# Optimization experiments

Measured on AMD Instinct MI355X. Metric: run time of the kernel, lower is better.

## Reference

```python
import jax, jax.numpy as jnp
import numpy as np

N, D, H = 16384, 128, 512
C = 1.0          # curvature c_in
EPS_GIN = 0.0    # GIN epsilon
MIN_NORM = 1e-7


def _arcosh(z):
    z = jnp.clip(z, 1.0 + MIN_NORM, None)
    return jnp.log(z + jnp.sqrt(z * z - 1.0))


def exp_map_zero(u, c):
    # hyperboloid exp at origin; tangent 'time' coord u[...,0] is ignored
    sqrtK = 1.0 / jnp.sqrt(c)
    x = u[..., 1:]
    n = jnp.clip(jnp.linalg.norm(x, axis=-1, keepdims=True), MIN_NORM, None)
    theta = n / sqrtK
    return jnp.concatenate(
        [sqrtK * jnp.cosh(theta), sqrtK * jnp.sinh(theta) * x / n], axis=-1)


def log_map_zero(p, c):
    # hyperboloid log at origin; result has zero 'time' coord
    sqrtK = 1.0 / jnp.sqrt(c)
    y = p[..., 1:]
    n = jnp.clip(jnp.linalg.norm(y, axis=-1, keepdims=True), MIN_NORM, None)
    theta = _arcosh(p[..., :1] / sqrtK)
    return jnp.concatenate(
        [jnp.zeros_like(theta), sqrtK * theta * y / n], axis=-1)


def setup_inputs() -> dict:
    key = jax.random.key(0)
    k1, k2, k3, k4 = jax.random.split(key, 4)
    x = jax.random.normal(k1, (N, D), dtype=jnp.float32)
    adj = jax.random.uniform(k2, (N, N), dtype=jnp.float32) / N  # row-normalized-ish
    W1 = jax.random.normal(k3, (D, H), dtype=jnp.float32) * (1.0 / np.sqrt(D))
    b1 = jnp.zeros((H,), dtype=jnp.float32)
    W2 = jax.random.normal(k4, (H, D), dtype=jnp.float32) * (1.0 / np.sqrt(H))
    b2 = jnp.zeros((D,), dtype=jnp.float32)
    return {"x": x, "adj": adj, "W1": W1, "b1": b1, "W2": W2, "b2": b2}


def reference(x, adj, W1, b1, W2, b2):
    # 1) lift features onto hyperboloid
    h = exp_map_zero(x, C)                       # [N, D]
    # 2) LorentzAgg (no attention): aggregate in tangent space at origin
    agg = exp_map_zero(adj @ log_map_zero(h, C), C)   # [N, D]
    # 3) GIN combine in tangent space: log(out) + (1+eps)*log(x_r), then exp
    out = exp_map_zero(log_map_zero(agg, C) + (1.0 + EPS_GIN) * log_map_zero(h, C), C)
    # 4) GIN MLP
    t = jax.nn.relu(out @ W1 + b1) @ W2 + b2     # [N, D]
    return t
```

## Files before the change

### kernel.cpp

```cpp
#include <hip/hip_runtime.h>

#define GN 16384
#define GD 128
#define GH 512
#define GK 16384

#define SPLITS 4
#define SKK (GK / SPLITS)
#define BM 128
#define BK 64

typedef __attribute__((ext_vector_type(8))) short s8v;
typedef __attribute__((ext_vector_type(4))) float f4v;
typedef __attribute__((ext_vector_type(4))) int   i4v;

#define AS1 __attribute__((address_space(1)))
#define AS3 __attribute__((address_space(3)))

static __device__ inline unsigned short f2bf(float f) {
  union { float f; unsigned u; } a; a.f = f;
  unsigned r = a.u + 0x7fffu + ((a.u >> 16) & 1u);
  return (unsigned short)(r >> 16);
}

static __device__ inline unsigned cvtpk(float lo, float hi) {
  unsigned r;
  asm("v_cvt_pk_bf16_f32 %0, %1, %2" : "=v"(r) : "v"(lo), "v"(hi));
  return r;
}

static __device__ inline float waveAllSum(float v) {
  #pragma unroll
  for (int off = 32; off; off >>= 1) v += __shfl_xor(v, off);
  return v;
}

__global__ void k_logmap(const float* __restrict__ x, float* __restrict__ Lf) {
  int row  = (blockIdx.x << 2) + (threadIdx.x >> 6);
  int lane = threadIdx.x & 63;
  size_t base = ((size_t)row << 7) + (lane << 1);
  float2 v = *(const float2*)(x + base);
  float a0 = (lane == 0) ? 0.f : v.x;
  float a1 = v.y;
  float n = fmaxf(sqrtf(waveAllSum(a0*a0 + a1*a1)), 1e-7f);
  float sh = sinhf(n), ch = coshf(n);
  float y0 = sh * a0 / n, y1 = sh * a1 / n;
  float ny = fmaxf(sqrtf(waveAllSum(y0*y0 + y1*y1)), 1e-7f);
  float z  = fmaxf(ch, 1.f + 1e-7f);
  float th = logf(z + sqrtf(z*z - 1.f));
  float l0 = th * y0 / ny;
  float l1 = th * y1 / ny;
  if (lane == 0) l0 = 0.f;
  *(float2*)(Lf + base) = make_float2(l0, l1);
}

__global__ void k_tconv(const float* __restrict__ src, unsigned short* __restrict__ dst,
                        int NR, int NC) {
  __shared__ float tile[64][65];
  const int r0 = blockIdx.x << 6;
  const int c0 = blockIdx.y << 6;
  const int t  = threadIdx.x;
  const int r  = t >> 2;
  const int cg = (t & 3) << 4;
  const float* s = src + (size_t)(r0 + r) * NC + c0 + cg;
  #pragma unroll
  for (int j = 0; j < 4; ++j) {
    float4 f = ((const float4*)s)[j];
    tile[r][cg + 4*j + 0] = f.x;
    tile[r][cg + 4*j + 1] = f.y;
    tile[r][cg + 4*j + 2] = f.z;
    tile[r][cg + 4*j + 3] = f.w;
  }
  __syncthreads();
  s8v o0, o1;
  #pragma unroll
  for (int j = 0; j < 8; ++j) o0[j] = (short)f2bf(tile[cg + j][r]);
  #pragma unroll
  for (int j = 0; j < 8; ++j) o1[j] = (short)f2bf(tile[cg + 8 + j][r]);
  unsigned short* d = dst + (size_t)(c0 + r) * NR + r0 + cg;
  *(s8v*)d = o0;
  *((s8v*)d + 1) = o1;
}

__global__ __launch_bounds__(512) void k_gemm(const float* __restrict__ adj,
    const unsigned short* __restrict__ Lt, float* __restrict__ Mpart) {
  __shared__ __align__(16) float          As[BM * BK];
  __shared__ __align__(16) unsigned short Bs[128 * BK];
  const int tid  = threadIdx.x;
  const int lane = tid & 63, wid = tid >> 6;
  const int wr = wid >> 2, wn = wid & 3;
  const int l15 = lane & 15, lhi = (lane >> 4) << 3;
  const int bid = blockIdx.x;
  const int split = bid & 3, rowblk = bid >> 2;
  const size_t blockRow = (size_t)rowblk * BM;
  const size_t k0 = (size_t)split * SKK;

  f4v acc[4][2];
  #pragma unroll
  for (int m = 0; m < 4; ++m)
    #pragma unroll
    for (int n = 0; n < 2; ++n) acc[m][n] = (f4v){0.f, 0.f, 0.f, 0.f};

  const int rA = tid >> 4, gA = tid & 15;
  const float* aSrc = adj + (blockRow + rA) * (size_t)GK + k0
                      + (size_t)((gA ^ (rA & 7)) << 2);
  const int rB = tid >> 3, gB = tid & 7;
  const unsigned short* bSrc = Lt + (size_t)rB * GK + k0
                               + (size_t)((gB ^ (rB & 7)) << 3);

  char* AsB = (char*)As;
  char* BsB = (char*)Bs;

  const int NIT = SKK / BK;
  for (int it = 0; it < NIT; ++it) {
    const float*          ap = aSrc + (size_t)it * BK;
    const unsigned short* bp = bSrc + (size_t)it * BK;
    #pragma unroll
    for (int j = 0; j < 4; ++j)
      __builtin_amdgcn_global_load_lds(
        (const AS1 void*)(ap + (size_t)j * 32 * GK),
        (AS3 void*)(AsB + ((tid + j * 512) << 4)), 16, 0, 0);
    #pragma unroll
    for (int j = 0; j < 2; ++j)
      __builtin_amdgcn_global_load_lds(
        (const AS1 void*)(bp + (size_t)j * 64 * GK),
        (AS3 void*)(BsB + ((tid + j * 512) << 4)), 16, 0, 0);
    __syncthreads();

    #pragma unroll
    for (int ks = 0; ks < 2; ++ks) {
      s8v bfr[2];
      #pragma unroll
      for (int n = 0; n < 2; ++n) {
        int rowb = 32*wn + 16*n + l15;
        int gb   = (4*ks + (lhi >> 3)) ^ (rowb & 7);
        bfr[n] = *(const s8v*)(BsB + rowb * 128 + (gb << 4));
      }
      #pragma unroll
      for (int m = 0; m < 4; ++m) {
        int rowa = 64*wr + 16*m + l15;
        int ga0  = 8*ks + (lhi >> 2);
        int sw   = rowa & 7;
        f4v x0 = *(const f4v*)(AsB + rowa * 256 + ((ga0       ^ sw) << 4));
        f4v x1 = *(const f4v*)(AsB + rowa * 256 + (((ga0 + 1) ^ sw) << 4));
        union { unsigned u[4]; s8v v; } ua;
        ua.u[0] = cvtpk(x0[0], x0[1]);
        ua.u[1] = cvtpk(x0[2], x0[3]);
        ua.u[2] = cvtpk(x1[0], x1[1]);
        ua.u[3] = cvtpk(x1[2], x1[3]);
        acc[m][0] = __builtin_amdgcn_mfma_f32_16x16x32_bf16(ua.v, bfr[0], acc[m][0], 0, 0, 0);
        acc[m][1] = __builtin_amdgcn_mfma_f32_16x16x32_bf16(ua.v, bfr[1], acc[m][1], 0, 0, 0);
      }
    }
    __syncthreads();
  }

  float* mp = Mpart + (size_t)split * GN * GD;
  #pragma unroll
  for (int m = 0; m < 4; ++m)
    #pragma unroll
    for (int n = 0; n < 2; ++n) {
      size_t r0 = blockRow + 64*wr + 16*m + ((lane >> 4) << 2);
      int    c0 = 32*wn + 16*n + l15;
      #pragma unroll
      for (int j = 0; j < 4; ++j)
        mp[(r0 + j) * GD + c0] = acc[m][n][j];
    }
}

__global__ void k_maps(const float* __restrict__ Mp, const float* __restrict__ Lf,
                       unsigned short* __restrict__ outB) {
  int row  = (blockIdx.x << 2) + (threadIdx.x >> 6);
  int lane = threadIdx.x & 63;
  size_t base = ((size_t)row << 7) + (lane << 1);
  const size_t PS = (size_t)GN * GD;
  float2 m0 = *(const float2*)(Mp + base);
  float2 m1 = *(const float2*)(Mp + PS + base);
  float2 m2 = *(const float2*)(Mp + 2*PS + base);
  float2 m3 = *(const float2*)(Mp + 3*PS + base);
  float mvx = (m0.x + m1.x) + (m2.x + m3.x);
  float mvy = (m0.y + m1.y) + (m2.y + m3.y);
  float2 lv = *(const float2*)(Lf + base);
  float v0 = (lane == 0) ? 0.f : mvx;
  float v1 = mvy;
  float nv = fmaxf(sqrtf(waveAllSum(v0*v0 + v1*v1)), 1e-7f);
  float ch = coshf(nv), sh = sinhf(nv);
  float g0 = sh * v0 / nv, g1 = sh * v1 / nv;
  float ny = fmaxf(sqrtf(waveAllSum(g0*g0 + g1*g1)), 1e-7f);
  float z  = fmaxf(ch, 1.f + 1e-7f);
  float th = logf(z + sqrtf(z*z - 1.f));
  float la0 = th * g0 / ny, la1 = th * g1 / ny;
  float s0 = la0 + lv.x, s1 = la1 + lv.y;
  if (lane == 0) s0 = 0.f;
  float ns  = fmaxf(sqrtf(waveAllSum(s0*s0 + s1*s1)), 1e-7f);
  float ch2 = coshf(ns), sh2 = sinhf(ns);
  float o0 = sh2 * s0 / ns, o1 = sh2 * s1 / ns;
  if (lane == 0) o0 = ch2;
  unsigned pack = (unsigned)f2bf(o0) | ((unsigned)f2bf(o1) << 16);
  *(unsigned*)(outB + base) = pack;
}

#define PAD1 136
#define PADH 520
__global__ __launch_bounds__(256, 2) void k_mlp(const unsigned short* __restrict__ outB,
    const unsigned short* __restrict__ W1t, const float* __restrict__ b1,
    const unsigned short* __restrict__ W2t, const float* __restrict__ b2,
    float* __restrict__ Tout) {
  __shared__ __align__(16) short sA[32 * PAD1];
  __shared__ __align__(16) short sH[32 * PADH];
  const int tid  = threadIdx.x;
  const int lane = tid & 63, wc = tid >> 6;
  const int row0 = blockIdx.x << 5;

  {
    const int r = tid >> 3, cg = (tid & 7) << 4;
    const unsigned short* src = outB + (size_t)(row0 + r) * GD + cg;
    i4v v0 = ((const i4v*)src)[0];
    i4v v1 = ((const i4v*)src)[1];
    *(i4v*)&sA[r * PAD1 + cg]     = v0;
    *(i4v*)&sA[r * PAD1 + cg + 8] = v1;
  }
  __syncthreads();

  f4v acc1[2][8];
  #pragma unroll
  for (int mi = 0; mi < 2; ++mi)
    #pragma unroll
    for (int ni = 0; ni < 8; ++ni) acc1[mi][ni] = (f4v){0.f,0.f,0.f,0.f};

  const int afr = (lane & 15) * PAD1 + ((lane >> 4) << 3);
  #pragma unroll
  for (int kk = 0; kk < 4; ++kk) {
    s8v a0 = *(const s8v*)&sA[afr + kk*32];
    s8v a1 = *(const s8v*)&sA[afr + 16*PAD1 + kk*32];
    #pragma unroll
    for (int ni = 0; ni < 8; ++ni) {
      const unsigned short* bp = W1t + (size_t)(128*wc + 16*ni + (lane & 15)) * GD
                                 + ((lane >> 4) << 3) + kk*32;
      s8v b = *(const s8v*)bp;
      acc1[0][ni] = __builtin_amdgcn_mfma_f32_16x16x32_bf16(a0, b, acc1[0][ni], 0, 0, 0);
      acc1[1][ni] = __builtin_amdgcn_mfma_f32_16x16x32_bf16(a1, b, acc1[1][ni], 0, 0, 0);
    }
  }
  #pragma unroll
  for (int ni = 0; ni < 8; ++ni) {
    int col = 128*wc + 16*ni + (lane & 15);
    float bb = b1[col];
    #pragma unroll
    for (int mi = 0; mi < 2; ++mi) {
      #pragma unroll
      for (int j = 0; j < 4; ++j) {
        int row = 16*mi + ((lane >> 4) << 2) + j;
        float v = fmaxf(acc1[mi][ni][j] + bb, 0.f);
        sH[row * PADH + col] = (short)f2bf(v);
      }
    }
  }
  __syncthreads();

  f4v acc2[2][2];
  #pragma unroll
  for (int mi = 0; mi < 2; ++mi)
    #pragma unroll
    for (int ni = 0; ni < 2; ++ni) acc2[mi][ni] = (f4v){0.f,0.f,0.f,0.f};

  const int hfr = (lane & 15) * PADH + ((lane >> 4) << 3);
  #pragma unroll
  for (int kk = 0; kk < 16; ++kk) {
    s8v a0 = *(const s8v*)&sH[hfr + kk*32];
    s8v a1 = *(const s8v*)&sH[hfr + 16*PADH + kk*32];
    #pragma unroll
    for (int ni = 0; ni < 2; ++ni) {
      const unsigned short* bp = W2t + (size_t)(32*wc + 16*ni + (lane & 15)) * GH
                                 + ((lane >> 4) << 3) + kk*32;
      s8v b = *(const s8v*)bp;
      acc2[0][ni] = __builtin_amdgcn_mfma_f32_16x16x32_bf16(a0, b, acc2[0][ni], 0, 0, 0);
      acc2[1][ni] = __builtin_amdgcn_mfma_f32_16x16x32_bf16(a1, b, acc2[1][ni], 0, 0, 0);
    }
  }
  #pragma unroll
  for (int mi = 0; mi < 2; ++mi)
    #pragma unroll
    for (int ni = 0; ni < 2; ++ni) {
      int c0 = 32*wc + 16*ni + (lane & 15);
      float bb = b2[c0];
      size_t r0 = row0 + 16*mi + ((lane >> 4) << 2);
      #pragma unroll
      for (int j = 0; j < 4; ++j)
        Tout[(r0 + j) * GD + c0] = acc2[mi][ni][j] + bb;
    }
}

extern "C" void kernel_launch(void* const* d_in, const int* in_sizes, int n_in,
                              void* d_out, int out_size, void* d_ws, size_t ws_size,
                              hipStream_t stream) {
  const float* x   = (const float*)d_in[0];
  const float* adj = (const float*)d_in[1];
  const float* W1  = (const float*)d_in[2];
  const float* b1  = (const float*)d_in[3];
  const float* W2  = (const float*)d_in[4];
  const float* b2  = (const float*)d_in[5];
  float* Tout = (float*)d_out;

  char* ws = (char*)d_ws;
  float*          Lf    = (float*)ws;
  unsigned short* Lt    = (unsigned short*)(ws + (8u  << 20));
  float*          Mpart = (float*)(ws + (12u << 20));
  unsigned short* outB  = (unsigned short*)(ws + (44u << 20));
  unsigned short* W1t   = (unsigned short*)(ws + (48u << 20));
  unsigned short* W2t   = (unsigned short*)(ws + (48u << 20) + (128u << 10));

  k_logmap <<<GN / 4, 256, 0, stream>>>(x, Lf);
  k_tconv  <<<dim3(GK / 64, GD / 64), 256, 0, stream>>>(Lf, Lt, GN, GD);
  k_tconv  <<<dim3(GD / 64, GH / 64), 256, 0, stream>>>(W1, W1t, GD, GH);
  k_tconv  <<<dim3(GH / 64, GD / 64), 256, 0, stream>>>(W2, W2t, GH, GD);
  k_gemm   <<<(GN / BM) * SPLITS, 512, 0, stream>>>(adj, Lt, Mpart);
  k_maps   <<<GN / 4, 256, 0, stream>>>(Mpart, Lf, outB);
  k_mlp    <<<GN / 32, 256, 0, stream>>>(outB, W1t, b1, W2t, b2, Tout);
}
```

Before: 274.7 us.

## Double-buffer adjacency GEMM LDS stages with smaller row tiles and fewer K splits

The adj@L GEMM now uses two LDS buffers so global-to-LDS loads for the next K step are issued before computing the current one. Row tiles shrink from 128 to 64 and K splits drop from 4 to 2, keeping the block count while halving the partial-sum buffers written and reduced in the maps kernel. The trade-off is twice the reads of the transposed L matrix and higher LDS use per block, which may limit occupancy.

```diff
diff --git a/kernel.cpp b/kernel.cpp
--- a/kernel.cpp
+++ b/kernel.cpp
@@ -5,9 +5,9 @@
 #define GH 512
 #define GK 16384
 
-#define SPLITS 4
+#define SPLITS 2
 #define SKK (GK / SPLITS)
-#define BM 128
+#define BM 64
 #define BK 64
 
 typedef __attribute__((ext_vector_type(8))) short s8v;
@@ -82,22 +82,24 @@
   *((s8v*)d + 1) = o1;
 }
 
+#define ASZ (BM * BK * 4)
+#define BSZ (128 * BK * 2)
+#define BUFSZ (ASZ + BSZ)
 __global__ __launch_bounds__(512) void k_gemm(const float* __restrict__ adj,
     const unsigned short* __restrict__ Lt, float* __restrict__ Mpart) {
-  __shared__ __align__(16) float          As[BM * BK];
-  __shared__ __align__(16) unsigned short Bs[128 * BK];
+  __shared__ __align__(16) char lds[2 * BUFSZ];
   const int tid  = threadIdx.x;
   const int lane = tid & 63, wid = tid >> 6;
   const int wr = wid >> 2, wn = wid & 3;
   const int l15 = lane & 15, lhi = (lane >> 4) << 3;
   const int bid = blockIdx.x;
-  const int split = bid & 3, rowblk = bid >> 2;
+  const int split = bid & 1, rowblk = bid >> 1;
   const size_t blockRow = (size_t)rowblk * BM;
   const size_t k0 = (size_t)split * SKK;
 
-  f4v acc[4][2];
-  #pragma unroll
-  for (int m = 0; m < 4; ++m)
+  f4v acc[2][2];
+  #pragma unroll
+  for (int m = 0; m < 2; ++m)
     #pragma unroll
     for (int n = 0; n < 2; ++n) acc[m][n] = (f4v){0.f, 0.f, 0.f, 0.f};
 
@@ -108,25 +110,35 @@
   const unsigned short* bSrc = Lt + (size_t)rB * GK + k0
                                + (size_t)((gB ^ (rB & 7)) << 3);
 
-  char* AsB = (char*)As;
-  char* BsB = (char*)Bs;
-
   const int NIT = SKK / BK;
+
+#define STAGE(c, itv)                                                          \
+  {                                                                            \
+    const float*          ap = aSrc + (size_t)(itv) * BK;                      \
+    const unsigned short* bp = bSrc + (size_t)(itv) * BK;                      \
+    char* ab = lds + (c) * BUFSZ;                                              \
+    char* bb = lds + (c) * BUFSZ + ASZ;                                        \
+    _Pragma("unroll")                                                          \
+    for (int j = 0; j < 2; ++j)                                                \
+      __builtin_amdgcn_global_load_lds(                                        \
+        (const AS1 void*)(ap + (size_t)j * 32 * GK),                           \
+        (AS3 void*)(ab + ((tid + j * 512) << 4)), 16, 0, 0);                   \
+    _Pragma("unroll")                                                          \
+    for (int j = 0; j < 2; ++j)                                                \
+      __builtin_amdgcn_global_load_lds(                                        \
+        (const AS1 void*)(bp + (size_t)j * 64 * GK),                           \
+        (AS3 void*)(bb + ((tid + j * 512) << 4)), 16, 0, 0);                   \
+  }
+
+  int cur = 0;
+  STAGE(0, 0);
+  __syncthreads();
+
   for (int it = 0; it < NIT; ++it) {
-    const float*          ap = aSrc + (size_t)it * BK;
-    const unsigned short* bp = bSrc + (size_t)it * BK;
-    #pragma unroll
-    for (int j = 0; j < 4; ++j)
-      __builtin_amdgcn_global_load_lds(
-        (const AS1 void*)(ap + (size_t)j * 32 * GK),
-        (AS3 void*)(AsB + ((tid + j * 512) << 4)), 16, 0, 0);
-    #pragma unroll
-    for (int j = 0; j < 2; ++j)
-      __builtin_amdgcn_global_load_lds(
-        (const AS1 void*)(bp + (size_t)j * 64 * GK),
-        (AS3 void*)(BsB + ((tid + j * 512) << 4)), 16, 0, 0);
-    __syncthreads();
-
+    if (it + 1 < NIT) STAGE(cur ^ 1, it + 1);
+
+    const char* ab = lds + cur * BUFSZ;
+    const char* bb = lds + cur * BUFSZ + ASZ;
     #pragma unroll
     for (int ks = 0; ks < 2; ++ks) {
       s8v bfr[2];
@@ -134,15 +146,15 @@
       for (int n = 0; n < 2; ++n) {
         int rowb = 32*wn + 16*n + l15;
         int gb   = (4*ks + (lhi >> 3)) ^ (rowb & 7);
-        bfr[n] = *(const s8v*)(BsB + rowb * 128 + (gb << 4));
+        bfr[n] = *(const s8v*)(bb + rowb * 128 + (gb << 4));
       }
       #pragma unroll
-      for (int m = 0; m < 4; ++m) {
-        int rowa = 64*wr + 16*m + l15;
+      for (int m = 0; m < 2; ++m) {
+        int rowa = 32*wr + 16*m + l15;
         int ga0  = 8*ks + (lhi >> 2);
         int sw   = rowa & 7;
-        f4v x0 = *(const f4v*)(AsB + rowa * 256 + ((ga0       ^ sw) << 4));
-        f4v x1 = *(const f4v*)(AsB + rowa * 256 + (((ga0 + 1) ^ sw) << 4));
+        f4v x0 = *(const f4v*)(ab + rowa * 256 + ((ga0       ^ sw) << 4));
+        f4v x1 = *(const f4v*)(ab + rowa * 256 + (((ga0 + 1) ^ sw) << 4));
         union { unsigned u[4]; s8v v; } ua;
         ua.u[0] = cvtpk(x0[0], x0[1]);
         ua.u[1] = cvtpk(x0[2], x0[3]);
@@ -153,14 +165,16 @@
       }
     }
     __syncthreads();
-  }
+    cur ^= 1;
+  }
+#undef STAGE
 
   float* mp = Mpart + (size_t)split * GN * GD;
   #pragma unroll
-  for (int m = 0; m < 4; ++m)
+  for (int m = 0; m < 2; ++m)
     #pragma unroll
     for (int n = 0; n < 2; ++n) {
-      size_t r0 = blockRow + 64*wr + 16*m + ((lane >> 4) << 2);
+      size_t r0 = blockRow + 32*wr + 16*m + ((lane >> 4) << 2);
       int    c0 = 32*wn + 16*n + l15;
       #pragma unroll
       for (int j = 0; j < 4; ++j)
@@ -176,10 +190,8 @@
   const size_t PS = (size_t)GN * GD;
   float2 m0 = *(const float2*)(Mp + base);
   float2 m1 = *(const float2*)(Mp + PS + base);
-  float2 m2 = *(const float2*)(Mp + 2*PS + base);
-  float2 m3 = *(const float2*)(Mp + 3*PS + base);
-  float mvx = (m0.x + m1.x) + (m2.x + m3.x);
-  float mvy = (m0.y + m1.y) + (m2.y + m3.y);
+  float mvx = m0.x + m1.x;
+  float mvy = m0.y + m1.y;
   float2 lv = *(const float2*)(Lf + base);
   float v0 = (lane == 0) ? 0.f : mvx;
   float v1 = mvy;
@@ -306,9 +318,9 @@
   float*          Lf    = (float*)ws;
   unsigned short* Lt    = (unsigned short*)(ws + (8u  << 20));
   float*          Mpart = (float*)(ws + (12u << 20));
-  unsigned short* outB  = (unsigned short*)(ws + (44u << 20));
-  unsigned short* W1t   = (unsigned short*)(ws + (48u << 20));
-  unsigned short* W2t   = (unsigned short*)(ws + (48u << 20) + (128u << 10));
+  unsigned short* outB  = (unsigned short*)(ws + (28u << 20));
+  unsigned short* W1t   = (unsigned short*)(ws + (32u << 20));
+  unsigned short* W2t   = (unsigned short*)(ws + (32u << 20) + (128u << 10));
 
   k_logmap <<<GN / 4, 256, 0, stream>>>(x, Lf);
   k_tconv  <<<dim3(GK / 64, GD / 64), 256, 0, stream>>>(Lf, Lt, GN, GD);
```

After: 256.8 us (median of 3 runs). -6.5%, faster.
